# Optimization experiments

Measured on AMD Instinct MI355X. Metric: run time of the kernel, lower is better.

## Reference

```python
import jax, jax.numpy as jnp
import numpy as np

WORD_DIM = 200
ASPECT_DIM = 32
NUM_NEG = 2
AVG_RATING = 3.8
LR_RATING = 1.0
LR_ABAE = 1.0


def setup_inputs() -> dict:
    key = jax.random.key(0)
    ks = jax.random.split(key, 20)
    R, L, D, A, B, NNZ = 20000, 30, WORD_DIM, ASPECT_DIM, 4096, 65536
    e_w = jax.random.normal(ks[0], (R, L, D), jnp.float32)
    y_s = jax.random.normal(ks[1], (R, D), jnp.float32)
    z_n = jax.random.normal(ks[2], (R * NUM_NEG, D), jnp.float32)
    label = jax.random.uniform(ks[3], (B,), jnp.float32, 1.0, 5.0)
    u_idx = jnp.stack([jax.random.randint(ks[4], (NNZ,), 0, B),
                       jax.random.randint(ks[5], (NNZ,), 0, R)]).astype(jnp.int64)
    i_idx = jnp.stack([jax.random.randint(ks[6], (NNZ,), 0, B),
                       jax.random.randint(ks[7], (NNZ,), 0, R)]).astype(jnp.int64)
    u_val = jax.random.uniform(ks[8], (NNZ,), jnp.float32)
    i_val = jax.random.uniform(ks[9], (NNZ,), jnp.float32)
    s = 0.05
    M_w = jax.random.normal(ks[10], (D, D), jnp.float32) * s
    M_b = jnp.zeros((D,), jnp.float32)
    W_w = jax.random.normal(ks[11], (A, D), jnp.float32) * s
    W_b = jnp.zeros((A,), jnp.float32)
    T_w = jax.random.normal(ks[12], (D, A), jnp.float32) * s
    T_b = jnp.zeros((D,), jnp.float32)
    fc_w = jax.random.uniform(ks[13], (1, A), jnp.float32, -0.05, 0.05)
    fc_b = jnp.zeros((1,), jnp.float32)
    fm_V = jax.random.uniform(ks[14], (A, 10), jnp.float32, -0.05, 0.05)
    return dict(e_w=e_w, y_s=y_s, z_n=z_n, label=label,
                user_histor_value=u_val, item_histor_value=i_val,
                M_w=M_w, M_b=M_b, W_w=W_w, W_b=W_b, T_w=T_w, T_b=T_b,
                fc_w=fc_w, fc_b=fc_b, fm_V=fm_V,
                user_histor_index=u_idx, item_histor_index=i_idx)


def _l2norm(x, axis):
    return x / jnp.maximum(jnp.linalg.norm(x, axis=axis, keepdims=True), 1e-12)


def reference(e_w, y_s, z_n, label, user_histor_value, item_histor_value,
              M_w, M_b, W_w, W_b, T_w, T_b, fc_w, fc_b, fm_V,
              user_histor_index, item_histor_index):
    R, L, D = e_w.shape
    A = W_w.shape[0]
    B = label.shape[0]
    # ABAE attention: dx = (e_w @ M^T + b) . y_s  -> (R, L)
    Me = jnp.einsum('rld,ed->rle', e_w, M_w) + M_b  # (R, L, D)
    dx = jnp.einsum('rld,rd->rl', Me, y_s)
    ax = jax.nn.softmax(dx, axis=1)                 # attention over words
    z_s = jnp.einsum('rld,rl->rd', e_w, ax)         # (R, D) weighted sentence emb
    p_t = z_s @ W_w.T + W_b                         # (R, A) aspect weights
    r_s = p_t @ T_w.T + T_b                         # (R, D) reconstructed emb
    # margin ranking (hinge) loss on cosine similarities
    c1 = jnp.sum(_l2norm(r_s, 1) * _l2norm(z_s, 1), axis=-1, keepdims=True)  # (R,1)
    c1 = jnp.tile(c1, (1, NUM_NEG)).reshape(-1)                              # (R*neg,)
    zn = _l2norm(z_n.reshape(R, NUM_NEG, D), 2)
    c2 = jnp.sum(zn * _l2norm(r_s, 1)[:, None, :], axis=-1).reshape(-1)
    abae_out_loss = jnp.maximum(0.0, 1.0 - (c1 - c2))
    J_loss = jnp.mean(abae_out_loss)
    # orthogonality regularizer on aspect matrix columns
    Tn = _l2norm(T_w, 0)                            # normalize each column (dim=0)
    G = Tn.T @ Tn                                   # (A, A)
    U_loss = jnp.mean((G - jnp.eye(A, dtype=G.dtype)) ** 2)
    abae_loss = U_loss + J_loss
    # sparse pooling: (B, R) sparse @ (R, A)
    u_rows, u_cols = user_histor_index[0], user_histor_index[1]
    i_rows, i_cols = item_histor_index[0], item_histor_index[1]
    user_aspect = jax.ops.segment_sum(p_t[u_cols] * user_histor_value[:, None],
                                      u_rows, num_segments=B)
    item_aspect = jax.ops.segment_sum(p_t[i_cols] * item_histor_value[:, None],
                                      i_rows, num_segments=B)
    output_emb = user_aspect * item_aspect          # (B, A)
    # factorization machine
    fm_linear = output_emb @ fc_w.T + fc_b          # (B, 1)
    i1 = (output_emb @ fm_V) ** 2
    i2 = (output_emb ** 2) @ (fm_V ** 2)
    # NOTE: faithful to source -- the 0.5*sum reduces over ALL elements (scalar)
    fm_output = 0.5 * jnp.sum(i1 - i2) + fm_linear  # (B, 1)
    prediction = fm_output + jnp.float32(AVG_RATING)
    rating_out_loss = (prediction.reshape(-1) - label) ** 2
    rating_loss = jnp.mean(rating_out_loss)
    obj = LR_RATING * rating_loss + LR_ABAE * abae_loss
    return (obj, rating_out_loss, abae_out_loss, prediction, user_aspect, item_aspect)
```

## Files before the change

### kernel.cpp

```cpp
#include <hip/hip_runtime.h>
#include <hip/hip_bf16.h>
#include <math.h>

#define R_CNT   20000
#define L_CNT   30
#define D_CNT   200
#define A_CNT   32
#define B_CNT   4096
#define NNZ_CNT 65536
#define AVG_RATING 3.8f

#define NW 1536
#define BUCK_CAP 128

#define OUT_OBJ  0
#define OUT_RL   1
#define OUT_AB   (1 + B_CNT)
#define OUT_PRED (OUT_AB + 2*R_CNT)
#define OUT_UA   (OUT_PRED + B_CNT)
#define OUT_IA   (OUT_UA + B_CNT*A_CNT)

#define WS_MODE   32
#define WS_FMLIN  64
#define WS_PT     16448
#define WS_V      2576448
#define WS_JPART  18576448
#define WS_SFPART 18588736
#define WS_UPART  18605120
#define WS_CNT    18605248
#define WS_BUCK   18638016

#define WAITV(N) do { asm volatile("s_waitcnt vmcnt(" #N ")" ::: "memory"); \
                      __builtin_amdgcn_sched_barrier(0); } while (0)
#define SB0() __builtin_amdgcn_sched_barrier(0)
#define WAIT_ALL() do { asm volatile("s_waitcnt vmcnt(0) lgkmcnt(0)" ::: "memory"); \
                        __builtin_amdgcn_sched_barrier(0); } while (0)

__device__ __forceinline__ float4 blk_reduce4(float4 v, float4* scratch) {
    __syncthreads();
    #pragma unroll
    for (int o = 32; o >= 1; o >>= 1) {
        v.x += __shfl_xor(v.x, o);
        v.y += __shfl_xor(v.y, o);
        v.z += __shfl_xor(v.z, o);
        v.w += __shfl_xor(v.w, o);
    }
    int w = threadIdx.x >> 6;
    if ((threadIdx.x & 63) == 0) scratch[w] = v;
    __syncthreads();
    float4 t0 = scratch[0], t1 = scratch[1], t2 = scratch[2], t3 = scratch[3];
    return make_float4(t0.x + t1.x + t2.x + t3.x,
                       t0.y + t1.y + t2.y + t3.y,
                       t0.z + t1.z + t2.z + t3.z,
                       t0.w + t1.w + t2.w + t3.w);
}

__global__ __launch_bounds__(256) void k_pre(const float* __restrict__ y_s,
                                             const float* __restrict__ M_w,
                                             const float* __restrict__ T_w,
                                             const int* __restrict__ u_idx,
                                             float* __restrict__ V,
                                             float* __restrict__ upart,
                                             int* __restrict__ cnt,
                                             int* __restrict__ mode) {
    __shared__ __align__(16) float sh[8224];
    const int tid = threadIdx.x;
    const int bid = blockIdx.x;

    if (bid < 313) {
        float* Msh = sh;
        float* Ysh = sh + 6500;
        int r0 = bid * 64;
        int dg = tid & 31, rg = tid >> 5;
        float acc[8][8];
        #pragma unroll
        for (int i = 0; i < 8; i++)
            #pragma unroll
            for (int j = 0; j < 8; j++) acc[i][j] = 0.f;
        for (int e0 = 0; e0 < D_CNT; e0 += 25) {
            __syncthreads();
            for (int idx = tid; idx < 25 * 256; idx += 256) {
                int ee = idx >> 8, d = idx & 255;
                Msh[ee * 260 + d] = (d < D_CNT) ? M_w[(e0 + ee) * D_CNT + d] : 0.f;
            }
            for (int idx = tid; idx < 25 * 64; idx += 256) {
                int rr = idx / 25, ee = idx - rr * 25;
                int row = r0 + rr;
                Ysh[ee * 68 + rr] = (row < R_CNT) ? y_s[row * D_CNT + e0 + ee] : 0.f;
            }
            __syncthreads();
            for (int ee = 0; ee < 25; ee++) {
                const float4 ya = *(const float4*)&Ysh[ee * 68 + rg * 8];
                const float4 yb = *(const float4*)&Ysh[ee * 68 + rg * 8 + 4];
                const float4 ma = *(const float4*)&Msh[ee * 260 + dg * 8];
                const float4 mb = *(const float4*)&Msh[ee * 260 + dg * 8 + 4];
                float ys[8] = {ya.x, ya.y, ya.z, ya.w, yb.x, yb.y, yb.z, yb.w};
                float ms[8] = {ma.x, ma.y, ma.z, ma.w, mb.x, mb.y, mb.z, mb.w};
                #pragma unroll
                for (int i = 0; i < 8; i++)
                    #pragma unroll
                    for (int j = 0; j < 8; j++)
                        acc[i][j] = fmaf(ys[i], ms[j], acc[i][j]);
            }
        }
        if (dg < 25) {
            #pragma unroll
            for (int i = 0; i < 8; i++) {
                int row = r0 + rg * 8 + i;
                if (row < R_CNT) {
                    *(float4*)&V[row * D_CNT + dg * 8]     = make_float4(acc[i][0], acc[i][1], acc[i][2], acc[i][3]);
                    *(float4*)&V[row * D_CNT + dg * 8 + 4] = make_float4(acc[i][4], acc[i][5], acc[i][6], acc[i][7]);
                }
            }
        }
    } else if (bid < 345) {
        float* Tsh = sh;
        float* tn  = sh + 6400;
        float4* red4 = (float4*)(sh + 6448);
        for (int idx = tid; idx < 1600; idx += 256)
            ((float4*)Tsh)[idx] = ((const float4*)T_w)[idx];
        __syncthreads();
        int a = tid >> 3, k = tid & 7;
        float p = 0.f;
        #pragma unroll
        for (int j = 0; j < 25; ++j) { float t = Tsh[(k + 8*j)*32 + a]; p = fmaf(t, t, p); }
        p += __shfl_xor(p, 1); p += __shfl_xor(p, 2); p += __shfl_xor(p, 4);
        if (k == 0) tn[a] = fmaxf(sqrtf(p), 1e-12f);
        __syncthreads();
        const int i = bid - 313;
        float s = 0.f;
        #pragma unroll
        for (int j = 0; j < 25; ++j)
            s = fmaf(Tsh[(k + 8*j)*32 + i], Tsh[(k + 8*j)*32 + a], s);
        s += __shfl_xor(s, 1); s += __shfl_xor(s, 2); s += __shfl_xor(s, 4);
        float part = 0.f;
        if (k == 0) {
            float g = s / (tn[i] * tn[a]);
            float diff = g - ((i == a) ? 1.f : 0.f);
            part = diff * diff;
        }
        float4 tot = blk_reduce4(make_float4(part, 0.f, 0.f, 0.f), red4);
        if (tid == 0) upart[i] = tot.x;
    } else {
        #pragma unroll
        for (int j = 0; j < 32; ++j) cnt[j * 256 + tid] = 0;
        if (tid == 0) {
            int m = 1;
            for (int i = 1; i < 256; i += 2) if (u_idx[i] != 0) { m = 0; break; }
            *mode = m;
        }
    }
}

__global__ __launch_bounds__(256) void k_bucket(const int* __restrict__ u_idx,
                                                const int* __restrict__ i_idx,
                                                const float* __restrict__ u_val,
                                                const float* __restrict__ i_val,
                                                const int* __restrict__ mode,
                                                int* __restrict__ cnt,
                                                long long* __restrict__ buck) {
    int gid = blockIdx.x * 256 + threadIdx.x;
    int side = gid >= NNZ_CNT;
    int k = gid - (side ? NNZ_CNT : 0);
    const int* idx = side ? i_idx : u_idx;
    float val = (side ? i_val : u_val)[k];
    int m64 = *mode;
    int row, col;
    if (m64) { row = idx[2 * k]; col = idx[2 * (NNZ_CNT + k)]; }
    else     { row = idx[k];     col = idx[NNZ_CNT + k]; }
    int bin = side * B_CNT + row;
    int slot = atomicAdd(&cnt[bin], 1);
    if (slot < BUCK_CAP) {
        long long pk = (long long)(unsigned int)col |
                       ((long long)__float_as_int(val) << 32);
        buck[(size_t)bin * BUCK_CAP + slot] = pk;
    }
}

__device__ __forceinline__ void stage_chunk(const float* src, float* lds,
                                            int lane, const float* ew_last4) {
    #pragma unroll
    for (int i = 0; i < 12; ++i) {
        const float* p = src + i * 256 + lane * 4;
        if (p > ew_last4) p = ew_last4;
        __builtin_amdgcn_global_load_lds(
            (const __attribute__((address_space(1))) unsigned int*)p,
            (__attribute__((address_space(3))) unsigned int*)(lds + i * 256),
            16, 0, 0);
    }
}
__device__ __forceinline__ void stage_v(const float* vsrc, float* lds, int lane) {
    #pragma unroll
    for (int i = 0; i < 4; ++i)
        __builtin_amdgcn_global_load_lds(
            (const __attribute__((address_space(1))) unsigned int*)(vsrc + i * 64 + lane),
            (__attribute__((address_space(3))) unsigned int*)(lds + i * 64),
            4, 0, 0);
}

__device__ __forceinline__ void chunk_pass(const float* __restrict__ eb,
                                           const float* __restrict__ vb,
                                           float* __restrict__ dxs,
                                           int lane, float& m, float& s,
                                           float4& zacc) {
    int l = lane >> 2, k = lane & 3;
    float p = 0.f;
    if (l < 15) {
        const float4* er = (const float4*)(eb + l * 200);
        const float4* vr = (const float4*)vb;
        #pragma unroll
        for (int t = 0; t < 13; ++t) {
            int idx = k + 4 * t;
            if (idx < 50) {
                float4 e = er[idx], v = vr[idx];
                p += e.x * v.x + e.y * v.y + e.z * v.z + e.w * v.w;
            }
        }
    }
    p += __shfl_xor(p, 1);
    p += __shfl_xor(p, 2);
    if (l < 15 && k == 0) dxs[l] = p;
    float4 d0 = ((const float4*)dxs)[0];
    float4 d1 = ((const float4*)dxs)[1];
    float4 d2 = ((const float4*)dxs)[2];
    float4 d3 = ((const float4*)dxs)[3];
    float dx[15] = {d0.x, d0.y, d0.z, d0.w, d1.x, d1.y, d1.z, d1.w,
                    d2.x, d2.y, d2.z, d2.w, d3.x, d3.y, d3.z};
    float cm = dx[0];
    #pragma unroll
    for (int q = 1; q < 15; ++q) cm = fmaxf(cm, dx[q]);
    float mn = fmaxf(m, cm);
    float sc = __expf(m - mn);
    float w[15];
    float ss = 0.f;
    #pragma unroll
    for (int q = 0; q < 15; ++q) { w[q] = __expf(dx[q] - mn); ss += w[q]; }
    s = s * sc + ss;
    zacc.x *= sc; zacc.y *= sc; zacc.z *= sc; zacc.w *= sc;
    if (lane < 50) {
        #pragma unroll
        for (int q = 0; q < 15; ++q) {
            float4 e = ((const float4*)(eb + q * 200))[lane];
            zacc.x = fmaf(w[q], e.x, zacc.x);
            zacc.y = fmaf(w[q], e.y, zacc.y);
            zacc.z = fmaf(w[q], e.z, zacc.z);
            zacc.w = fmaf(w[q], e.w, zacc.w);
        }
    }
    m = mn;
}

__global__ __launch_bounds__(64) void k_zs(const float* __restrict__ e_w,
                                           const float* __restrict__ V,
                                           const float* __restrict__ z_n,
                                           const float* __restrict__ W_w,
                                           const float* __restrict__ W_b,
                                           const float* __restrict__ T_w,
                                           const float* __restrict__ T_b,
                                           float* __restrict__ p_t,
                                           float* __restrict__ out,
                                           double* __restrict__ jpart) {
    __shared__ __align__(16) float bufE[2][3072];
    __shared__ __align__(16) float bufV[2][256];
    const int lane = threadIdx.x;
    const bool act = lane < 50;
    const int dl = act ? lane : 0;
    const float* ew_last4 = e_w + (size_t)R_CNT * 6000 - 4;

    const float wb = W_b[lane >> 1];
    float4 tbv = make_float4(0.f, 0.f, 0.f, 0.f);
    if (act) tbv = ((const float4*)T_b)[dl];
    float tb[4] = {tbv.x, tbv.y, tbv.z, tbv.w};

    double jloc = 0.0;
    int rev = blockIdx.x;
    stage_v(V + (size_t)rev * 200, bufV[0], lane);
    stage_chunk(e_w + (size_t)rev * 6000, bufE[0], lane, ew_last4);
    int pv = 0;
    for (;;) {
        int rnext = rev + NW;
        bool last = (rnext >= R_CNT);
        int rc = last ? rev : rnext;
        float m = -3.0e38f, s = 0.f;
        float4 zacc = make_float4(0.f, 0.f, 0.f, 0.f);
        SB0();
        stage_chunk(e_w + (size_t)rev * 6000 + 3000, bufE[1], lane, ew_last4);
        stage_v(V + (size_t)rc * 200, bufV[pv ^ 1], lane);
        float4 zn0 = make_float4(0.f, 0.f, 0.f, 0.f);
        float4 zn1 = make_float4(0.f, 0.f, 0.f, 0.f);
        if (act) {
            zn0 = ((const float4*)(z_n + (size_t)(2 * rev) * 200))[lane];
            zn1 = ((const float4*)(z_n + (size_t)(2 * rev + 1) * 200))[lane];
        }
        WAITV(18);
        chunk_pass(bufE[0], bufV[pv], bufV[pv] + 208, lane, m, s, zacc);
        SB0();
        stage_chunk(e_w + (size_t)rc * 6000, bufE[0], lane, ew_last4);
        WAITV(18);
        chunk_pass(bufE[1], bufV[pv], bufV[pv] + 208, lane, m, s, zacc);

        float* zsh  = bufE[1];
        float* ptsL = bufE[1] + 208;
        const float inv = 1.f / s;
        float zf[4] = {zacc.x * inv, zacc.y * inv, zacc.z * inv, zacc.w * inv};
        if (act) ((float4*)zsh)[dl] = make_float4(zf[0], zf[1], zf[2], zf[3]);

        {
            int a = lane >> 1, half = lane & 1;
            const float4* wrow = (const float4*)(W_w + a * 200);
            const float4* zrow = (const float4*)zsh;
            float p = 0.f;
            #pragma unroll
            for (int t = 0; t < 25; ++t) {
                int idx = half + 2 * t;
                float4 wv = wrow[idx];
                float4 zv = zrow[idx];
                p += wv.x * zv.x + wv.y * zv.y + wv.z * zv.z + wv.w * zv.w;
            }
            p += __shfl_xor(p, 1);
            float pt = p + wb;
            if (half == 0) {
                ptsL[a] = pt;
                p_t[(size_t)rev * 32 + a] = pt;
            }
        }

        float rr = 0.f, rz = 0.f, zz = 0.f, n00 = 0.f, n0r = 0.f, n11 = 0.f, n1r = 0.f;
        {
            const float4* pt4 = (const float4*)ptsL;
            float4 pq0 = pt4[0], pq1 = pt4[1], pq2 = pt4[2], pq3 = pt4[3];
            float4 pq4 = pt4[4], pq5 = pt4[5], pq6 = pt4[6], pq7 = pt4[7];
            if (act) {
                float znf0[4] = {zn0.x, zn0.y, zn0.z, zn0.w};
                float znf1[4] = {zn1.x, zn1.y, zn1.z, zn1.w};
                #pragma unroll
                for (int j = 0; j < 4; ++j) {
                    int d = 4 * dl + j;
                    const float4* trow = (const float4*)(T_w + d * 32);
                    float r = tb[j];
                    float4 t0 = trow[0], t1 = trow[1], t2 = trow[2], t3 = trow[3];
                    float4 t4 = trow[4], t5 = trow[5], t6 = trow[6], t7 = trow[7];
                    r += t0.x*pq0.x + t0.y*pq0.y + t0.z*pq0.z + t0.w*pq0.w;
                    r += t1.x*pq1.x + t1.y*pq1.y + t1.z*pq1.z + t1.w*pq1.w;
                    r += t2.x*pq2.x + t2.y*pq2.y + t2.z*pq2.z + t2.w*pq2.w;
                    r += t3.x*pq3.x + t3.y*pq3.y + t3.z*pq3.z + t3.w*pq3.w;
                    r += t4.x*pq4.x + t4.y*pq4.y + t4.z*pq4.z + t4.w*pq4.w;
                    r += t5.x*pq5.x + t5.y*pq5.y + t5.z*pq5.z + t5.w*pq5.w;
                    r += t6.x*pq6.x + t6.y*pq6.y + t6.z*pq6.z + t6.w*pq6.w;
                    r += t7.x*pq7.x + t7.y*pq7.y + t7.z*pq7.z + t7.w*pq7.w;
                    rr  += r * r;
                    rz  += r * zf[j];
                    zz  += zf[j] * zf[j];
                    n00 += znf0[j] * znf0[j];
                    n0r += znf0[j] * r;
                    n11 += znf1[j] * znf1[j];
                    n1r += znf1[j] * r;
                }
            }
        }
        #pragma unroll
        for (int o = 1; o < 64; o <<= 1) {
            rr  += __shfl_xor(rr, o);  rz  += __shfl_xor(rz, o);
            zz  += __shfl_xor(zz, o);  n00 += __shfl_xor(n00, o);
            n0r += __shfl_xor(n0r, o); n11 += __shfl_xor(n11, o);
            n1r += __shfl_xor(n1r, o);
        }
        if (lane == 0) {
            float nr = fmaxf(sqrtf(rr), 1e-12f);
            float nz = fmaxf(sqrtf(zz), 1e-12f);
            float c1  = rz  / (nr * nz);
            float c20 = n0r / (fmaxf(sqrtf(n00), 1e-12f) * nr);
            float c21 = n1r / (fmaxf(sqrtf(n11), 1e-12f) * nr);
            float l0 = fmaxf(0.f, 1.f - (c1 - c20));
            float l1 = fmaxf(0.f, 1.f - (c1 - c21));
            out[OUT_AB + 2 * rev]     = l0;
            out[OUT_AB + 2 * rev + 1] = l1;
            jloc += (double)l0 + (double)l1;
        }
        if (last) break;
        rev = rnext;
        pv ^= 1;
    }
    if (lane == 0) jpart[blockIdx.x] = jloc;
}

__global__ __launch_bounds__(64) void k_rowsum_fm(const long long* __restrict__ buck,
                                                  const int* __restrict__ cnt,
                                                  const float* __restrict__ p_t,
                                                  const float* __restrict__ fc_w,
                                                  const float* __restrict__ fc_b,
                                                  const float* __restrict__ fm_V,
                                                  float* __restrict__ fm_lin,
                                                  float* __restrict__ sfpart,
                                                  float* __restrict__ out) {
    __shared__ long long ent[2][BUCK_CAP];
    const int lane = threadIdx.x;
    const int b = blockIdx.x;
    const int a = lane & 31;

    int n0 = cnt[b];          if (n0 > BUCK_CAP) n0 = BUCK_CAP;
    int n1 = cnt[B_CNT + b];  if (n1 > BUCK_CAP) n1 = BUCK_CAP;
    {
        const long long* s0 = buck + (size_t)b * BUCK_CAP;
        const long long* s1 = buck + (size_t)(B_CNT + b) * BUCK_CAP;
        if (lane < n0)      ent[0][lane]      = s0[lane];
        if (lane + 64 < n0) ent[0][lane + 64] = s0[lane + 64];
        if (lane < n1)      ent[1][lane]      = s1[lane];
        if (lane + 64 < n1) ent[1][lane + 64] = s1[lane + 64];
    }
    WAIT_ALL();

    float side_acc[2];
    const int h = lane >> 5;
    #pragma unroll
    for (int s = 0; s < 2; ++s) {
        int n = s ? n1 : n0;
        float acc = 0.f;
        for (int e = h; e < n; e += 2) {
            long long pk = ent[s][e];
            int col = (int)(unsigned int)(pk & 0xffffffffLL);
            float val = __int_as_float((int)(pk >> 32));
            acc = fmaf(p_t[(size_t)col * 32 + a], val, acc);
        }
        acc += __shfl_xor(acc, 32);
        side_acc[s] = acc;
        if (lane < 32)
            out[(s ? OUT_IA : OUT_UA) + b * 32 + lane] = acc;
    }

    float oe = side_acc[0] * side_acc[1];
    float oe2 = oe * oe;
    float lin = oe * fc_w[a];
    #pragma unroll
    for (int o = 1; o < 32; o <<= 1) lin += __shfl_xor(lin, o);
    float part = 0.f;
    #pragma unroll
    for (int j = 0; j < 10; ++j) {
        float v = fm_V[a * 10 + j];
        float s1 = oe * v;
        float s2 = oe2 * v * v;
        #pragma unroll
        for (int o = 1; o < 32; o <<= 1) { s1 += __shfl_xor(s1, o); s2 += __shfl_xor(s2, o); }
        part += s1 * s1 - s2;
    }
    if (lane == 0) {
        fm_lin[b] = lin + fc_b[0];
        sfpart[b] = 0.5f * part;
    }
}

__global__ __launch_bounds__(256) void k_predfinal(const float* __restrict__ label,
                                                   const float* __restrict__ fm_lin,
                                                   const float* __restrict__ sfpart,
                                                   const double* __restrict__ jpart,
                                                   const float* __restrict__ upart,
                                                   float* __restrict__ out) {
    __shared__ double dred[4];
    __shared__ float Ssh;
    __shared__ float ured[4];
    int tid = threadIdx.x;
    double sl = 0.0;
    #pragma unroll
    for (int i = 0; i < 16; ++i) sl += (double)sfpart[tid + 256 * i];
    #pragma unroll
    for (int o = 32; o >= 1; o >>= 1) sl += __shfl_xor(sl, o);
    if ((tid & 63) == 0) dred[tid >> 6] = sl;
    __syncthreads();
    if (tid == 0) Ssh = (float)(dred[0] + dred[1] + dred[2] + dred[3]);
    __syncthreads();
    float S = Ssh;
    double racc = 0.0;
    #pragma unroll
    for (int i = 0; i < 16; ++i) {
        int b = tid + 256 * i;
        float pred = fm_lin[b] + S + AVG_RATING;
        float d = pred - label[b];
        float rl = d * d;
        out[OUT_PRED + b] = pred;
        out[OUT_RL + b] = rl;
        racc += (double)rl;
    }
    double jacc = 0.0;
    for (int i = tid; i < NW; i += 256) jacc += jpart[i];
    float u = (tid < 32) ? upart[tid] : 0.f;
    #pragma unroll
    for (int o = 32; o >= 1; o >>= 1) {
        racc += __shfl_xor(racc, o);
        jacc += __shfl_xor(jacc, o);
        u    += __shfl_xor(u, o);
    }
    __syncthreads();
    if ((tid & 63) == 0) dred[tid >> 6] = racc;
    __syncthreads();
    double rsum = dred[0] + dred[1] + dred[2] + dred[3];
    __syncthreads();
    if ((tid & 63) == 0) dred[tid >> 6] = jacc;
    __syncthreads();
    double jsum = dred[0] + dred[1] + dred[2] + dred[3];
    if ((tid & 63) == 0) ured[tid >> 6] = u;
    __syncthreads();
    if (tid == 0) {
        double U = (double)(ured[0] + ured[1] + ured[2] + ured[3]) / 1024.0;
        double J = jsum / (2.0 * R_CNT);
        double RL = rsum / (double)B_CNT;
        out[OUT_OBJ] = (float)(RL + U + J);
    }
}

extern "C" void kernel_launch(void* const* d_in, const int* in_sizes, int n_in,
                              void* d_out, int out_size, void* d_ws, size_t ws_size,
                              hipStream_t stream) {
    const float* e_w   = (const float*)d_in[0];
    const float* y_s   = (const float*)d_in[1];
    const float* z_n   = (const float*)d_in[2];
    const float* label = (const float*)d_in[3];
    const float* u_val = (const float*)d_in[4];
    const float* i_val = (const float*)d_in[5];
    const float* M_w   = (const float*)d_in[6];
    const float* W_w   = (const float*)d_in[8];
    const float* W_b   = (const float*)d_in[9];
    const float* T_w   = (const float*)d_in[10];
    const float* T_b   = (const float*)d_in[11];
    const float* fc_w  = (const float*)d_in[12];
    const float* fc_b  = (const float*)d_in[13];
    const float* fm_V  = (const float*)d_in[14];
    const int*   u_idx = (const int*)d_in[15];
    const int*   i_idx = (const int*)d_in[16];

    float* out = (float*)d_out;
    char* ws = (char*)d_ws;
    int* mode     = (int*)(ws + WS_MODE);
    float* fm_lin = (float*)(ws + WS_FMLIN);
    float* p_t    = (float*)(ws + WS_PT);
    float* V      = (float*)(ws + WS_V);
    double* jpart = (double*)(ws + WS_JPART);
    float* sfpart = (float*)(ws + WS_SFPART);
    float* upart  = (float*)(ws + WS_UPART);
    int* cnt      = (int*)(ws + WS_CNT);
    long long* buck = (long long*)(ws + WS_BUCK);

    k_pre<<<346, 256, 0, stream>>>(y_s, M_w, T_w, u_idx, V, upart, cnt, mode);
    k_bucket<<<2 * NNZ_CNT / 256, 256, 0, stream>>>(u_idx, i_idx, u_val, i_val,
                                                    mode, cnt, buck);
    k_zs<<<NW, 64, 0, stream>>>(e_w, V, z_n, W_w, W_b, T_w, T_b, p_t, out, jpart);
    k_rowsum_fm<<<B_CNT, 64, 0, stream>>>(buck, cnt, p_t, fc_w, fc_b, fm_V,
                                          fm_lin, sfpart, out);
    k_predfinal<<<1, 256, 0, stream>>>(label, fm_lin, sfpart, jpart, upart, out);
}
```

Measured before the change: 327.3 us.

## Restructure ABAE attention kernel into two-wave blocks with three-chunk row pipeline

```diff
diff --git a/kernel.cpp b/kernel.cpp
--- a/kernel.cpp
+++ b/kernel.cpp
@@ -10,7 +10,7 @@
 #define NNZ_CNT 65536
 #define AVG_RATING 3.8f
 
-#define NW 1536
+#define NW 2000
 #define BUCK_CAP 128
 
 #define OUT_OBJ  0
@@ -25,10 +25,10 @@
 #define WS_PT     16448
 #define WS_V      2576448
 #define WS_JPART  18576448
-#define WS_SFPART 18588736
-#define WS_UPART  18605120
-#define WS_CNT    18605248
-#define WS_BUCK   18638016
+#define WS_SFPART 18592448
+#define WS_UPART  18608832
+#define WS_CNT    18609024
+#define WS_BUCK   18641920
 
 #define WAITV(N) do { asm volatile("s_waitcnt vmcnt(" #N ")" ::: "memory"); \
                       __builtin_amdgcn_sched_barrier(0); } while (0)
@@ -177,10 +177,10 @@
     }
 }
 
-__device__ __forceinline__ void stage_chunk(const float* src, float* lds,
-                                            int lane, const float* ew_last4) {
-    #pragma unroll
-    for (int i = 0; i < 12; ++i) {
+__device__ __forceinline__ void stage_chunk8(const float* src, float* lds,
+                                             int lane, const float* ew_last4) {
+    #pragma unroll
+    for (int i = 0; i < 8; ++i) {
         const float* p = src + i * 256 + lane * 4;
         if (p > ew_last4) p = ew_last4;
         __builtin_amdgcn_global_load_lds(
@@ -198,14 +198,14 @@
             4, 0, 0);
 }
 
-__device__ __forceinline__ void chunk_pass(const float* __restrict__ eb,
-                                           const float* __restrict__ vb,
-                                           float* __restrict__ dxs,
-                                           int lane, float& m, float& s,
-                                           float4& zacc) {
+__device__ __forceinline__ void chunk_pass10(const float* __restrict__ eb,
+                                             const float* __restrict__ vb,
+                                             float* __restrict__ dxs,
+                                             int lane, float& m, float& s,
+                                             float4& zacc) {
     int l = lane >> 2, k = lane & 3;
     float p = 0.f;
-    if (l < 15) {
+    if (l < 10) {
         const float4* er = (const float4*)(eb + l * 200);
         const float4* vr = (const float4*)vb;
         #pragma unroll
@@ -219,27 +219,25 @@
     }
     p += __shfl_xor(p, 1);
     p += __shfl_xor(p, 2);
-    if (l < 15 && k == 0) dxs[l] = p;
+    if (l < 10 && k == 0) dxs[l] = p;
     float4 d0 = ((const float4*)dxs)[0];
     float4 d1 = ((const float4*)dxs)[1];
-    float4 d2 = ((const float4*)dxs)[2];
-    float4 d3 = ((const float4*)dxs)[3];
-    float dx[15] = {d0.x, d0.y, d0.z, d0.w, d1.x, d1.y, d1.z, d1.w,
-                    d2.x, d2.y, d2.z, d2.w, d3.x, d3.y, d3.z};
+    float2 d2 = ((const float2*)dxs)[4];
+    float dx[10] = {d0.x, d0.y, d0.z, d0.w, d1.x, d1.y, d1.z, d1.w, d2.x, d2.y};
     float cm = dx[0];
     #pragma unroll
-    for (int q = 1; q < 15; ++q) cm = fmaxf(cm, dx[q]);
+    for (int q = 1; q < 10; ++q) cm = fmaxf(cm, dx[q]);
     float mn = fmaxf(m, cm);
     float sc = __expf(m - mn);
-    float w[15];
+    float w[10];
     float ss = 0.f;
     #pragma unroll
-    for (int q = 0; q < 15; ++q) { w[q] = __expf(dx[q] - mn); ss += w[q]; }
+    for (int q = 0; q < 10; ++q) { w[q] = __expf(dx[q] - mn); ss += w[q]; }
     s = s * sc + ss;
     zacc.x *= sc; zacc.y *= sc; zacc.z *= sc; zacc.w *= sc;
     if (lane < 50) {
         #pragma unroll
-        for (int q = 0; q < 15; ++q) {
+        for (int q = 0; q < 10; ++q) {
             float4 e = ((const float4*)(eb + q * 200))[lane];
             zacc.x = fmaf(w[q], e.x, zacc.x);
             zacc.y = fmaf(w[q], e.y, zacc.y);
@@ -250,19 +248,21 @@
     m = mn;
 }
 
-__global__ __launch_bounds__(64) void k_zs(const float* __restrict__ e_w,
-                                           const float* __restrict__ V,
-                                           const float* __restrict__ z_n,
-                                           const float* __restrict__ W_w,
-                                           const float* __restrict__ W_b,
-                                           const float* __restrict__ T_w,
-                                           const float* __restrict__ T_b,
-                                           float* __restrict__ p_t,
-                                           float* __restrict__ out,
-                                           double* __restrict__ jpart) {
-    __shared__ __align__(16) float bufE[2][3072];
-    __shared__ __align__(16) float bufV[2][256];
-    const int lane = threadIdx.x;
+__global__ __launch_bounds__(128, 2) void k_zs(const float* __restrict__ e_w,
+                                               const float* __restrict__ V,
+                                               const float* __restrict__ z_n,
+                                               const float* __restrict__ W_w,
+                                               const float* __restrict__ W_b,
+                                               const float* __restrict__ T_w,
+                                               const float* __restrict__ T_b,
+                                               float* __restrict__ p_t,
+                                               float* __restrict__ out,
+                                               double* __restrict__ jpart) {
+    __shared__ __align__(16) float bufE[2][2][2048];
+    __shared__ __align__(16) float bufV[2][2][256];
+    const int lane = threadIdx.x & 63;
+    const int wv = threadIdx.x >> 6;
+    const int wave = blockIdx.x * 2 + wv;
     const bool act = lane < 50;
     const int dl = act ? lane : 0;
     const float* ew_last4 = e_w + (size_t)R_CNT * 6000 - 4;
@@ -273,34 +273,46 @@
     float tb[4] = {tbv.x, tbv.y, tbv.z, tbv.w};
 
     double jloc = 0.0;
-    int rev = blockIdx.x;
-    stage_v(V + (size_t)rev * 200, bufV[0], lane);
-    stage_chunk(e_w + (size_t)rev * 6000, bufE[0], lane, ew_last4);
-    int pv = 0;
-    for (;;) {
-        int rnext = rev + NW;
-        bool last = (rnext >= R_CNT);
-        int rc = last ? rev : rnext;
-        float m = -3.0e38f, s = 0.f;
-        float4 zacc = make_float4(0.f, 0.f, 0.f, 0.f);
+    const int rev0 = wave * 10;
+    stage_chunk8(e_w + (size_t)rev0 * 6000, bufE[wv][0], lane, ew_last4);
+    stage_v(V + (size_t)rev0 * 200, bufV[wv][0], lane);
+    int pb = 0, pv = 0;
+
+    #pragma unroll 1
+    for (int i = 0; i < 10; ++i) {
+        const int rev = rev0 + i;
+        int rn = rev + 1; if (rn >= R_CNT) rn = rev;
+        float* eA = bufE[wv][pb];
+        float* eB = bufE[wv][pb ^ 1];
+        float* vC = bufV[wv][pv];
+        float* vN = bufV[wv][pv ^ 1];
+        float* dxs = vC + 208;
+        const float* ew_r = e_w + (size_t)rev * 6000;
+
         SB0();
-        stage_chunk(e_w + (size_t)rev * 6000 + 3000, bufE[1], lane, ew_last4);
-        stage_v(V + (size_t)rc * 200, bufV[pv ^ 1], lane);
+        stage_chunk8(ew_r + 2000, eB, lane, ew_last4);
         float4 zn0 = make_float4(0.f, 0.f, 0.f, 0.f);
         float4 zn1 = make_float4(0.f, 0.f, 0.f, 0.f);
         if (act) {
             zn0 = ((const float4*)(z_n + (size_t)(2 * rev) * 200))[lane];
             zn1 = ((const float4*)(z_n + (size_t)(2 * rev + 1) * 200))[lane];
         }
-        WAITV(18);
-        chunk_pass(bufE[0], bufV[pv], bufV[pv] + 208, lane, m, s, zacc);
+        WAITV(10);
+        float m = -3.0e38f, s = 0.f;
+        float4 zacc = make_float4(0.f, 0.f, 0.f, 0.f);
+        chunk_pass10(eA, vC, dxs, lane, m, s, zacc);
         SB0();
-        stage_chunk(e_w + (size_t)rc * 6000, bufE[0], lane, ew_last4);
-        WAITV(18);
-        chunk_pass(bufE[1], bufV[pv], bufV[pv] + 208, lane, m, s, zacc);
-
-        float* zsh  = bufE[1];
-        float* ptsL = bufE[1] + 208;
+        stage_chunk8(ew_r + 4000, eA, lane, ew_last4);
+        WAITV(10);
+        chunk_pass10(eB, vC, dxs, lane, m, s, zacc);
+        SB0();
+        stage_chunk8(e_w + (size_t)rn * 6000, eB, lane, ew_last4);
+        stage_v(V + (size_t)rn * 200, vN, lane);
+        WAITV(12);
+        chunk_pass10(eA, vC, dxs, lane, m, s, zacc);
+
+        float* zsh  = eA;
+        float* ptsL = eA + 208;
         const float inv = 1.f / s;
         float zf[4] = {zacc.x * inv, zacc.y * inv, zacc.z * inv, zacc.w * inv};
         if (act) ((float4*)zsh)[dl] = make_float4(zf[0], zf[1], zf[2], zf[3]);
@@ -313,9 +325,9 @@
             #pragma unroll
             for (int t = 0; t < 25; ++t) {
                 int idx = half + 2 * t;
-                float4 wv = wrow[idx];
-                float4 zv = zrow[idx];
-                p += wv.x * zv.x + wv.y * zv.y + wv.z * zv.z + wv.w * zv.w;
+                float4 wv4 = wrow[idx];
+                float4 zv4 = zrow[idx];
+                p += wv4.x * zv4.x + wv4.y * zv4.y + wv4.z * zv4.z + wv4.w * zv4.w;
             }
             p += __shfl_xor(p, 1);
             float pt = p + wb;
@@ -377,11 +389,9 @@
             out[OUT_AB + 2 * rev + 1] = l1;
             jloc += (double)l0 + (double)l1;
         }
-        if (last) break;
-        rev = rnext;
-        pv ^= 1;
-    }
-    if (lane == 0) jpart[blockIdx.x] = jloc;
+        pb ^= 1; pv ^= 1;
+    }
+    if (lane == 0) jpart[wave] = jloc;
 }
 
 __global__ __launch_bounds__(64) void k_rowsum_fm(const long long* __restrict__ buck,
@@ -542,7 +552,7 @@
     k_pre<<<346, 256, 0, stream>>>(y_s, M_w, T_w, u_idx, V, upart, cnt, mode);
     k_bucket<<<2 * NNZ_CNT / 256, 256, 0, stream>>>(u_idx, i_idx, u_val, i_val,
                                                     mode, cnt, buck);
-    k_zs<<<NW, 64, 0, stream>>>(e_w, V, z_n, W_w, W_b, T_w, T_b, p_t, out, jpart);
+    k_zs<<<NW / 2, 128, 0, stream>>>(e_w, V, z_n, W_w, W_b, T_w, T_b, p_t, out, jpart);
     k_rowsum_fm<<<B_CNT, 64, 0, stream>>>(buck, cnt, p_t, fc_w, fc_b, fm_V,
                                           fm_lin, sfpart, out);
     k_predfinal<<<1, 256, 0, stream>>>(label, fm_lin, sfpart, jpart, upart, out);
```

Result: no change. 330.3 us (+0.9%).
